# Kernel optimization log

Measured on AMD Instinct MI355X. Metric: run time of the kernel, lower is better.

The kernel has to match this reference:

```python
import jax, jax.numpy as jnp
import numpy as np
import math

N, E = 1000, 128000
IN_DIM, HID, OUT_DIM = 256, 512, 16
L, H = 6, 8
C = HID // H  # 64, TransformerConv out_channels per head
EDGE_DIM = 32
MAX_LEN = 1000


def _pe(max_len, d_model):
    pos = np.arange(max_len)[:, None].astype(np.float32)
    div = np.exp(np.arange(0, d_model, 2).astype(np.float32) * (-math.log(10000.0) / d_model))
    pe = np.zeros((max_len, d_model), dtype=np.float32)
    pe[:, 0::2] = np.sin(pos * div)
    pe[:, 1::2] = np.cos(pos * div)
    return jnp.asarray(pe)


def setup_inputs() -> dict:
    key = jax.random.key(0)
    ks = jax.random.split(key, 32)
    g = lambda k, shape, fan_in: jax.random.normal(k, shape, jnp.float32) / jnp.sqrt(jnp.float32(fan_in))
    inp = {
        "x": jax.random.normal(ks[0], (N, IN_DIM), jnp.float32),
        "edge_index": jax.random.randint(ks[1], (2, E), 0, N, jnp.int64 if jax.config.jax_enable_x64 else jnp.int32),
        "edge_attr": jax.random.uniform(ks[2], (E, 4), jnp.float32),
        "embed_w": g(ks[3], (IN_DIM, HID), IN_DIM),
        "embed_b": jnp.zeros((HID,), jnp.float32),
        "pe": _pe(MAX_LEN, HID),
        "ee_w1": g(ks[4], (4, 16), 4), "ee_b1": jnp.zeros((16,), jnp.float32),
        "ee_w2": g(ks[5], (16, EDGE_DIM), 16), "ee_b2": jnp.zeros((EDGE_DIM,), jnp.float32),
        "q_w": g(ks[6], (L, HID, HID), HID), "q_b": jnp.zeros((L, HID), jnp.float32),
        "k_w": g(ks[7], (L, HID, HID), HID), "k_b": jnp.zeros((L, HID), jnp.float32),
        "v_w": g(ks[8], (L, HID, HID), HID), "v_b": jnp.zeros((L, HID), jnp.float32),
        "e_w": g(ks[9], (L, EDGE_DIM, HID), EDGE_DIM),
        "skip_w": g(ks[10], (L, HID, HID), HID), "skip_b": jnp.zeros((L, HID), jnp.float32),
        "ln_g": jnp.ones((L, HID), jnp.float32), "ln_b": jnp.zeros((L, HID), jnp.float32),
        "dom_w": g(ks[11], (HID, 16), HID), "dom_b": jnp.zeros((16,), jnp.float32),
        "cls_w1": g(ks[12], (HID + 16, HID // 2), HID + 16), "cls_b1": jnp.zeros((HID // 2,), jnp.float32),
        "cls_w2": g(ks[13], (HID // 2, OUT_DIM), HID // 2), "cls_b2": jnp.zeros((OUT_DIM,), jnp.float32),
    }
    return inp


def _layer_norm(x, g, b, eps=1e-5):
    mu = jnp.mean(x, axis=-1, keepdims=True)
    var = jnp.var(x, axis=-1, keepdims=True)
    return (x - mu) * jax.lax.rsqrt(var + eps) * g + b


def _forward(x, edge_index, edge_attr, embed_w, embed_b, pe, ee_w1, ee_b1, ee_w2, ee_b2,
             q_w, q_b, k_w, k_b, v_w, v_b, e_w, skip_w, skip_b, ln_g, ln_b,
             dom_w, dom_b, cls_w1, cls_b1, cls_w2, cls_b2):
    n = x.shape[0]
    h = x @ embed_w + embed_b
    h = h + pe[:n]
    # edge encoder: 4 -> 16 -> 32
    ef = jax.nn.relu(edge_attr @ ee_w1 + ee_b1) @ ee_w2 + ee_b2  # [E, 32]
    src, tgt = edge_index[0], edge_index[1]
    scale = 1.0 / math.sqrt(C)
    for l in range(L):
        res = h
        q = (h @ q_w[l] + q_b[l]).reshape(n, H, C)
        k = (h @ k_w[l] + k_b[l]).reshape(n, H, C)
        v = (h @ v_w[l] + v_b[l]).reshape(n, H, C)
        e = (ef @ e_w[l]).reshape(-1, H, C)            # [E, H, C], lin_edge has no bias
        kj = k[src] + e                                 # gather + edge bias
        score = jnp.sum(q[tgt] * kj, axis=-1) * scale   # [E, H]
        # segment softmax over incoming edges of each target node
        m = jax.ops.segment_max(score, tgt, num_segments=n)     # [N, H]
        al = jnp.exp(score - m[tgt])
        den = jax.ops.segment_sum(al, tgt, num_segments=n)      # [N, H]
        al = al / den[tgt]
        msg = (v[src] + e) * al[:, :, None]             # [E, H, C]
        out = jax.ops.segment_sum(msg, tgt, num_segments=n).reshape(n, HID)
        out = out + h @ skip_w[l] + skip_b[l]           # root_weight skip
        h = _layer_norm(out + res, ln_g[l], ln_b[l])
    dom = h @ dom_w + dom_b                             # [N, 16]
    comb = jnp.concatenate([h, dom], axis=-1)
    hid = jax.nn.relu(comb @ cls_w1 + cls_b1)
    return hid @ cls_w2 + cls_b2


def reference(x, edge_index, edge_attr, embed_w, embed_b, pe, ee_w1, ee_b1, ee_w2, ee_b2,
              q_w, q_b, k_w, k_b, v_w, v_b, e_w, skip_w, skip_b, ln_g, ln_b,
              dom_w, dom_b, cls_w1, cls_b1, cls_w2, cls_b2):
    return _forward(x, edge_index, edge_attr, embed_w, embed_b, pe, ee_w1, ee_b1, ee_w2, ee_b2,
                    q_w, q_b, k_w, k_b, v_w, v_b, e_w, skip_w, skip_b, ln_g, ln_b,
                    dom_w, dom_b, cls_w1, cls_b1, cls_w2, cls_b2)
```

## Files before the change

### kernel.cpp

```cpp
#include <hip/hip_runtime.h>
#include <hip/hip_bf16.h>
#include <cstdint>
#include <cstddef>

#define NN 1000
#define EE 128000
#define LAYERS 6
#define SCALE 0.125f
#define MAXDEG 320

typedef __attribute__((ext_vector_type(4))) float f32x4;
typedef __attribute__((ext_vector_type(8))) short short8v;

static __device__ __forceinline__ unsigned short f2bf(float x){
    unsigned int u = __float_as_uint(x);
    unsigned int lsb = (u >> 16) & 1u;
    u += 0x7fffu + lsb;
    return (unsigned short)(u >> 16);
}
static __device__ __forceinline__ float bf2f(unsigned short u){
    return __uint_as_float(((unsigned int)u) << 16);
}

__global__ void zero_counts(int* cnt){
    cnt[threadIdx.x] = 0;
}

__global__ void hist_kernel(const int* __restrict__ tgt, int* cnt){
    int e = blockIdx.x*256 + threadIdx.x;
    if (e < EE) atomicAdd(&cnt[tgt[e]], 1);
}

__global__ void scan_kernel(const int* __restrict__ cnt, int* offs, int* cursor){
    __shared__ int s[1024];
    int tid = threadIdx.x;
    s[tid] = (tid < NN) ? cnt[tid] : 0;
    __syncthreads();
    for (int st = 1; st < 1024; st <<= 1){
        int v = (tid >= st) ? s[tid-st] : 0;
        __syncthreads();
        s[tid] += v;
        __syncthreads();
    }
    int excl = (tid == 0) ? 0 : s[tid-1];
    if (tid < NN){ offs[tid] = excl; cursor[tid] = excl; }
    if (tid == 0) offs[NN] = s[NN-1];
}

__global__ void scatter_kernel(const int* __restrict__ src, const int* __restrict__ tgt,
                               int* cursor, int* ssrc, int* epos){
    int e = blockIdx.x*256 + threadIdx.x;
    if (e < EE){
        int t = tgt[e];
        int pos = atomicAdd(&cursor[t], 1);
        ssrc[pos] = src[e];
        epos[e] = pos;
    }
}

__global__ __launch_bounds__(256) void edge_enc(
    const float* __restrict__ edge_attr,
    const float* __restrict__ w1, const float* __restrict__ b1,
    const float* __restrict__ w2, const float* __restrict__ b2,
    const int* __restrict__ epos,
    unsigned short* __restrict__ efs)
{
    __shared__ float w1s[64], b1s[16], w2s[512], b2s[32];
    int tid = threadIdx.x;
    if (tid < 64) w1s[tid] = w1[tid];
    if (tid < 16) b1s[tid] = b1[tid];
    if (tid < 32) b2s[tid] = b2[tid];
    w2s[tid] = w2[tid];
    w2s[tid+256] = w2[tid+256];
    __syncthreads();
    int e = blockIdx.x*256 + tid;
    if (e >= EE) return;
    float4 av = *(const float4*)(edge_attr + (size_t)e*4);
    float hd[16];
    #pragma unroll
    for (int i = 0; i < 16; i++){
        float v = av.x*w1s[i] + av.y*w1s[16+i] + av.z*w1s[32+i] + av.w*w1s[48+i] + b1s[i];
        hd[i] = fmaxf(v, 0.f);
    }
    unsigned short* op = efs + (size_t)epos[e]*32;
    #pragma unroll
    for (int k4 = 0; k4 < 8; k4++){
        ushort4 ub;
        float v0 = b2s[k4*4+0], v1 = b2s[k4*4+1], v2 = b2s[k4*4+2], v3 = b2s[k4*4+3];
        #pragma unroll
        for (int i = 0; i < 16; i++){
            float hv = hd[i];
            v0 += hv*w2s[i*32 + k4*4+0];
            v1 += hv*w2s[i*32 + k4*4+1];
            v2 += hv*w2s[i*32 + k4*4+2];
            v3 += hv*w2s[i*32 + k4*4+3];
        }
        ub.x = f2bf(v0); ub.y = f2bf(v1); ub.z = f2bf(v2); ub.w = f2bf(v3);
        *(ushort4*)(op + k4*4) = ub;
    }
}

__global__ __launch_bounds__(256) void convert_all(
    const float* __restrict__ Wq, const float* __restrict__ Wk,
    const float* __restrict__ Wv, const float* __restrict__ Ws,
    const float* __restrict__ embed_w, const float* __restrict__ x,
    unsigned short* __restrict__ Wt, unsigned short* __restrict__ ewt,
    unsigned short* __restrict__ xb)
{
    int bid = blockIdx.x;
    int tid = threadIdx.x;
    if (bid < 6144){
        int mm = bid >> 8;
        int tile = bid & 255;
        int tk = tile >> 4, tn = tile & 15;
        int l = mm >> 2, m = mm & 3;
        const float* W = ((m==0)?Wq:(m==1)?Wk:(m==2)?Wv:Ws) + (size_t)l*512*512;
        unsigned short* dst = Wt + (size_t)mm*512*512;
        __shared__ float ts[32][33];
        int r = tid >> 3, c0 = (tid & 7)*4;
        float4 v = *(const float4*)(W + (size_t)(tk*32 + r)*512 + tn*32 + c0);
        ts[r][c0+0] = v.x; ts[r][c0+1] = v.y; ts[r][c0+2] = v.z; ts[r][c0+3] = v.w;
        __syncthreads();
        ushort4 o;
        o.x = f2bf(ts[c0+0][r]); o.y = f2bf(ts[c0+1][r]);
        o.z = f2bf(ts[c0+2][r]); o.w = f2bf(ts[c0+3][r]);
        *(ushort4*)(dst + (size_t)(tn*32 + r)*512 + tk*32 + c0) = o;
    } else if (bid < 6144 + 128){
        int tile = bid - 6144;
        int tn = tile & 15, tk = tile >> 4;
        __shared__ float ts2[32][33];
        int r = tid >> 3, c0 = (tid & 7)*4;
        float4 v = *(const float4*)(embed_w + (size_t)(tk*32 + r)*512 + tn*32 + c0);
        ts2[r][c0+0] = v.x; ts2[r][c0+1] = v.y; ts2[r][c0+2] = v.z; ts2[r][c0+3] = v.w;
        __syncthreads();
        ushort4 o;
        o.x = f2bf(ts2[c0+0][r]); o.y = f2bf(ts2[c0+1][r]);
        o.z = f2bf(ts2[c0+2][r]); o.w = f2bf(ts2[c0+3][r]);
        *(ushort4*)(ewt + (size_t)(tn*32 + r)*256 + tk*32 + c0) = o;
    } else {
        int row = bid - 6144 - 128;
        xb[(size_t)row*256 + tid] = (row < NN) ? f2bf(x[(size_t)row*256 + tid]) : (unsigned short)0;
    }
}

__global__ __launch_bounds__(256) void gemm_embed_mfma(
    const unsigned short* __restrict__ xb,
    const unsigned short* __restrict__ ewt,
    const float* __restrict__ bias, const float* __restrict__ pe,
    float* __restrict__ C, unsigned short* __restrict__ hb)
{
    int bid = blockIdx.x;
    int mt = bid >> 2, nt = bid & 3;
    int row0 = mt*64, col0 = nt*128;

    __shared__ __align__(16) unsigned short As[64*40];
    __shared__ __align__(16) unsigned short Bs[128*40];

    int tid = threadIdx.x;
    int wid = tid >> 6, l = tid & 63;
    int wm = wid >> 1, wn = wid & 1;

    f32x4 acc[2][4] = {};
    int ar = tid >> 2, akq = tid & 3;
    for (int k0 = 0; k0 < 256; k0 += 32){
        *(uint4*)&As[ar*40 + akq*8]      = *(const uint4*)&xb[(size_t)(row0+ar)*256 + k0 + akq*8];
        *(uint4*)&Bs[ar*40 + akq*8]      = *(const uint4*)&ewt[(size_t)(col0+ar)*256 + k0 + akq*8];
        *(uint4*)&Bs[(ar+64)*40 + akq*8] = *(const uint4*)&ewt[(size_t)(col0+ar+64)*256 + k0 + akq*8];
        __syncthreads();
        short8v a0 = *(const short8v*)&As[(wm*32 + (l&15))*40 + (l>>4)*8];
        short8v a1 = *(const short8v*)&As[(wm*32 + 16 + (l&15))*40 + (l>>4)*8];
        #pragma unroll
        for (int nj = 0; nj < 4; nj++){
            short8v b = *(const short8v*)&Bs[(wn*64 + nj*16 + (l&15))*40 + (l>>4)*8];
            acc[0][nj] = __builtin_amdgcn_mfma_f32_16x16x32_bf16(a0, b, acc[0][nj], 0, 0, 0);
            acc[1][nj] = __builtin_amdgcn_mfma_f32_16x16x32_bf16(a1, b, acc[1][nj], 0, 0, 0);
        }
        __syncthreads();
    }
    int rbase = (l >> 4)*4, cl = l & 15;
    #pragma unroll
    for (int mi = 0; mi < 2; mi++)
        #pragma unroll
        for (int nj = 0; nj < 4; nj++)
            #pragma unroll
            for (int r = 0; r < 4; r++){
                int grow = row0 + wm*32 + mi*16 + rbase + r;
                int gcol = col0 + wn*64 + nj*16 + cl;
                if (grow < NN){
                    float v = acc[mi][nj][r] + bias[gcol] + pe[(size_t)grow*512 + gcol];
                    C[(size_t)grow*512 + gcol] = v;
                    hb[(size_t)grow*512 + gcol] = f2bf(v);
                }
            }
}

__global__ __launch_bounds__(256) void gemm_qkvs_mfma(
    const unsigned short* __restrict__ hb,
    const unsigned short* __restrict__ Wt,
    const float* __restrict__ qb, const float* __restrict__ kb,
    const float* __restrict__ vb, const float* __restrict__ sb,
    float* __restrict__ Q, unsigned short* __restrict__ K16,
    unsigned short* __restrict__ V16, float* __restrict__ S)
{
    int bid = blockIdx.x;
    int mat = bid >> 7;
    int rem = bid & 127;
    int mt = rem >> 3, nt = rem & 7;
    int row0 = mt*64, col0 = nt*64;
    const unsigned short* W = Wt + (size_t)mat*512*512;
    const float* bias = (mat==0)?qb:(mat==1)?kb:(mat==2)?vb:sb;

    __shared__ __align__(16) unsigned short As[64*72];
    __shared__ __align__(16) unsigned short Bs[64*72];

    int tid = threadIdx.x;
    int wid = tid >> 6, l = tid & 63;
    int wm = wid >> 1, wn = wid & 1;

    f32x4 acc[2][2] = {};
    int lr = tid >> 2;
    int lc = (tid & 3)*2;
    const unsigned short* ga = hb + (size_t)(row0+lr)*512 + lc*8;
    const unsigned short* gb = W  + (size_t)(col0+lr)*512 + lc*8;

    uint4 ra0 = *(const uint4*)(ga);
    uint4 ra1 = *(const uint4*)(ga + 8);
    uint4 rb0 = *(const uint4*)(gb);
    uint4 rb1 = *(const uint4*)(gb + 8);

    for (int k0 = 0; k0 < 512; k0 += 64){
        __syncthreads();
        *(uint4*)&As[lr*72 + lc*8]     = ra0;
        *(uint4*)&As[lr*72 + lc*8 + 8] = ra1;
        *(uint4*)&Bs[lr*72 + lc*8]     = rb0;
        *(uint4*)&Bs[lr*72 + lc*8 + 8] = rb1;
        __syncthreads();
        if (k0 + 64 < 512){
            ra0 = *(const uint4*)(ga + k0 + 64);
            ra1 = *(const uint4*)(ga + k0 + 72);
            rb0 = *(const uint4*)(gb + k0 + 64);
            rb1 = *(const uint4*)(gb + k0 + 72);
        }
        #pragma unroll
        for (int ks = 0; ks < 2; ks++){
            short8v a0 = *(const short8v*)&As[(wm*32 + (l&15))*72      + ks*32 + (l>>4)*8];
            short8v a1 = *(const short8v*)&As[(wm*32 + 16 + (l&15))*72 + ks*32 + (l>>4)*8];
            short8v b0 = *(const short8v*)&Bs[(wn*32 + (l&15))*72      + ks*32 + (l>>4)*8];
            short8v b1 = *(const short8v*)&Bs[(wn*32 + 16 + (l&15))*72 + ks*32 + (l>>4)*8];
            acc[0][0] = __builtin_amdgcn_mfma_f32_16x16x32_bf16(a0, b0, acc[0][0], 0, 0, 0);
            acc[0][1] = __builtin_amdgcn_mfma_f32_16x16x32_bf16(a0, b1, acc[0][1], 0, 0, 0);
            acc[1][0] = __builtin_amdgcn_mfma_f32_16x16x32_bf16(a1, b0, acc[1][0], 0, 0, 0);
            acc[1][1] = __builtin_amdgcn_mfma_f32_16x16x32_bf16(a1, b1, acc[1][1], 0, 0, 0);
        }
    }
    int rbase = (l >> 4)*4, cl = l & 15;
    #pragma unroll
    for (int mi = 0; mi < 2; mi++)
        #pragma unroll
        for (int nj = 0; nj < 2; nj++)
            #pragma unroll
            for (int r = 0; r < 4; r++){
                int grow = row0 + wm*32 + mi*16 + rbase + r;
                int gcol = col0 + wn*32 + nj*16 + cl;
                if (grow < NN){
                    float v = acc[mi][nj][r] + bias[gcol];
                    if (mat == 0)      Q[(size_t)grow*512 + gcol] = v;
                    else if (mat == 1) K16[(size_t)grow*512 + gcol] = f2bf(v);
                    else if (mat == 2) V16[(size_t)grow*512 + gcol] = f2bf(v);
                    else               S[(size_t)grow*512 + gcol] = v;
                }
            }
}

__global__ __launch_bounds__(256) void attn_h4(
    const float* __restrict__ Qm, const unsigned short* __restrict__ Km,
    const unsigned short* __restrict__ Vm,
    const unsigned short* __restrict__ efs, const float* __restrict__ e_w_l,
    const int* __restrict__ ssrc, const int* __restrict__ offs,
    float* __restrict__ x_pre)
{
    int tid = threadIdx.x;
    int b = blockIdx.x;
    int t = b >> 1;
    int hh0 = (b & 1)*4;

    __shared__ float q_s[4*68];
    __shared__ float qe_s[4*36];
    __shared__ float sc_s[MAXDEG*4];
    __shared__ int   src_s[MAXDEG];
    __shared__ float pv_s[4*256];
    __shared__ float pe_s[4*128];
    __shared__ float s_s[128];
    __shared__ float red[16], red2[16];
    __shared__ float m_s[4], d_s[4];

    q_s[(tid>>6)*68 + (tid&63)] = Qm[(size_t)t*512 + hh0*64 + tid];
    __syncthreads();
    if (tid < 128){
        int h = tid >> 5, d = tid & 31;
        const float* wrow = e_w_l + (size_t)d*512 + (hh0+h)*64;
        const float* qh = q_s + h*68;
        float a = 0.f;
        #pragma unroll
        for (int c = 0; c < 64; c++) a += qh[c]*wrow[c];
        qe_s[h*36 + d] = a;
    }
    int start = offs[t], deg = offs[t+1] - start;
    __syncthreads();

    int cw = tid >> 5, l = tid & 31;
    int h = l >> 3, sub = l & 7;
    const float4* qp4  = (const float4*)(q_s + h*68 + sub*8);
    float4 qa0 = qp4[0], qa1 = qp4[1];
    float4 qev = *(const float4*)(qe_s + h*36 + sub*4);
    float lmax = -1e30f;
    #pragma unroll 2
    for (int i = cw; i < deg; i += 8){
        int s = ssrc[start + i];
        if (l == 0) src_s[i] = s;
        short8v kv = *(const short8v*)(Km + (size_t)s*512 + (hh0 + h)*64 + sub*8);
        ushort4 ev = *(const ushort4*)(efs + (size_t)(start+i)*32 + sub*4);
        float p;
        p  = qa0.x*bf2f((unsigned short)kv[0]) + qa0.y*bf2f((unsigned short)kv[1])
           + qa0.z*bf2f((unsigned short)kv[2]) + qa0.w*bf2f((unsigned short)kv[3]);
        p += qa1.x*bf2f((unsigned short)kv[4]) + qa1.y*bf2f((unsigned short)kv[5])
           + qa1.z*bf2f((unsigned short)kv[6]) + qa1.w*bf2f((unsigned short)kv[7]);
        p += qev.x*bf2f(ev.x) + qev.y*bf2f(ev.y)
           + qev.z*bf2f(ev.z) + qev.w*bf2f(ev.w);
        p += __shfl_xor(p, 1);
        p += __shfl_xor(p, 2);
        p += __shfl_xor(p, 4);
        p *= SCALE;
        lmax = fmaxf(lmax, p);
        if (sub == 0) sc_s[i*4 + h] = p;
    }
    lmax = fmaxf(lmax, __shfl_xor(lmax, 32));
    {
        int wl = tid & 63;
        if (wl < 32 && (wl & 7) == 0) red[(tid>>6)*4 + (wl>>3)] = lmax;
    }
    __syncthreads();
    if (tid < 4){
        float m = fmaxf(fmaxf(red[tid], red[4+tid]), fmaxf(red[8+tid], red[12+tid]));
        m_s[tid] = m;
    }
    __syncthreads();

    {
        int he = tid & 3, ie = tid >> 2;
        float mh = m_s[he];
        float den = 0.f;
        for (int i = ie; i < deg; i += 64){
            float al = __expf(sc_s[i*4 + he] - mh);
            sc_s[i*4 + he] = al;
            den += al;
        }
        den += __shfl_xor(den, 4);
        den += __shfl_xor(den, 8);
        den += __shfl_xor(den, 16);
        den += __shfl_xor(den, 32);
        if ((tid & 63) < 4) red2[(tid>>6)*4 + (tid & 3)] = den;
    }
    __syncthreads();
    if (tid < 4) d_s[tid] = red2[tid] + red2[4+tid] + red2[8+tid] + red2[12+tid];
    __syncthreads();

    {
        int g = tid >> 6, c4 = tid & 63;
        int h2 = c4 >> 4;
        int dp = (c4 & 15)*2;
        float4 accV = make_float4(0.f,0.f,0.f,0.f);
        float2 accE = make_float2(0.f,0.f);
        #pragma unroll 4
        for (int i = g; i < deg; i += 4){
            int s = src_s[i];
            float al = sc_s[i*4 + h2];
            ushort4 v = *(const ushort4*)(Vm + (size_t)s*512 + hh0*64 + c4*4);
            unsigned int e2 = *(const unsigned int*)(efs + (size_t)(start+i)*32 + dp);
            accV.x += al*bf2f(v.x); accV.y += al*bf2f(v.y);
            accV.z += al*bf2f(v.z); accV.w += al*bf2f(v.w);
            accE.x += al*bf2f((unsigned short)(e2 & 0xffffu));
            accE.y += al*bf2f((unsigned short)(e2 >> 16));
        }
        *(float4*)&pv_s[g*256 + c4*4] = accV;
        *(float2*)&pe_s[g*128 + c4*2] = accE;
    }
    __syncthreads();
    if (tid < 128){
        int h3 = tid >> 5, d = tid & 31;
        int c4s = h3*16 + (d >> 1), comp = d & 1;
        float dv = d_s[h3];
        float invd = (dv > 0.f) ? 1.f/dv : 0.f;
        float ssum = pe_s[c4s*2+comp] + pe_s[128 + c4s*2+comp]
                   + pe_s[256 + c4s*2+comp] + pe_s[384 + c4s*2+comp];
        s_s[h3*32 + d] = ssum * invd;
    }
    __syncthreads();

    int c = tid;
    int hh = c >> 6;
    float dv = d_s[hh];
    float invd = (dv > 0.f) ? 1.f/dv : 0.f;
    float vtot = pv_s[c] + pv_s[256+c] + pv_s[512+c] + pv_s[768+c];
    float r = vtot * invd;
    float oe = 0.f;
    const float* sp = s_s + hh*32;
    #pragma unroll
    for (int d = 0; d < 32; d++) oe += sp[d]*e_w_l[(size_t)d*512 + hh0*64 + c];
    x_pre[(size_t)t*512 + hh0*64 + c] = r + oe;
}

__global__ __launch_bounds__(256) void ln_skip(
    const float* __restrict__ x_pre, const float* __restrict__ SKm,
    const float* __restrict__ hcur,
    const float* __restrict__ ln_g_l, const float* __restrict__ ln_b_l,
    float* __restrict__ hnext, unsigned short* __restrict__ hbn)
{
    int tid = threadIdx.x, t = blockIdx.x;
    __shared__ float red[4], red2[4];
    float x0 = x_pre[(size_t)t*512 + tid]       + SKm[(size_t)t*512 + tid]       + hcur[(size_t)t*512 + tid];
    float x1 = x_pre[(size_t)t*512 + 256 + tid] + SKm[(size_t)t*512 + 256 + tid] + hcur[(size_t)t*512 + 256 + tid];
    float sA = x0 + x1, sB = x0*x0 + x1*x1;
    #pragma unroll
    for (int m = 1; m <= 32; m <<= 1){
        sA += __shfl_xor(sA, m);
        sB += __shfl_xor(sB, m);
    }
    int wv = tid >> 6, ln = tid & 63;
    if (ln == 0){ red[wv] = sA; red2[wv] = sB; }
    __syncthreads();
    float tot  = red[0] + red[1] + red[2] + red[3];
    float tot2 = red2[0] + red2[1] + red2[2] + red2[3];
    float mu  = tot*(1.f/512.f);
    float var = tot2*(1.f/512.f) - mu*mu;
    float rstd = rsqrtf(var + 1e-5f);
    float y0 = (x0 - mu)*rstd*ln_g_l[tid]     + ln_b_l[tid];
    float y1 = (x1 - mu)*rstd*ln_g_l[256+tid] + ln_b_l[256+tid];
    hnext[(size_t)t*512 + tid]       = y0;
    hnext[(size_t)t*512 + 256 + tid] = y1;
    hbn[(size_t)t*512 + tid]       = f2bf(y0);
    hbn[(size_t)t*512 + 256 + tid] = f2bf(y1);
}

__global__ __launch_bounds__(256) void final_head(
    const float* __restrict__ hin,
    const float* __restrict__ dom_w, const float* __restrict__ dom_b,
    const float* __restrict__ w1, const float* __restrict__ b1,
    const float* __restrict__ w2, const float* __restrict__ b2,
    float* __restrict__ out)
{
    int tid = threadIdx.x, t = blockIdx.x;
    __shared__ float h_s[512];
    __shared__ float dom_s[16];
    __shared__ float hid_s[256];
    __shared__ float red[256];
    h_s[tid]     = hin[(size_t)t*512 + tid];
    h_s[tid+256] = hin[(size_t)t*512 + 256 + tid];
    __syncthreads();
    if (tid < 16){
        float a = dom_b[tid];
        for (int i = 0; i < 512; i++) a += h_s[i]*dom_w[i*16 + tid];
        dom_s[tid] = a;
    }
    __syncthreads();
    float acc = b1[tid];
    for (int i = 0; i < 512; i++) acc += h_s[i]*w1[(size_t)i*256 + tid];
    #pragma unroll
    for (int i = 0; i < 16; i++) acc += dom_s[i]*w1[(size_t)(512+i)*256 + tid];
    hid_s[tid] = fmaxf(acc, 0.f);
    __syncthreads();
    int o = tid & 15, g = tid >> 4;
    float p = 0.f;
    #pragma unroll
    for (int j = 0; j < 16; j++) p += hid_s[g*16 + j]*w2[(g*16 + j)*16 + o];
    red[tid] = p;
    __syncthreads();
    if (tid < 16){
        float s2 = b2[tid];
        for (int gg = 0; gg < 16; gg++) s2 += red[gg*16 + tid];
        out[(size_t)t*16 + tid] = s2;
    }
}

extern "C" void kernel_launch(void* const* d_in, const int* in_sizes, int n_in,
                              void* d_out, int out_size, void* d_ws, size_t ws_size,
                              hipStream_t stream)
{
    const float* x       = (const float*)d_in[0];
    const int*   eidx    = (const int*)  d_in[1];
    const float* eattr   = (const float*)d_in[2];
    const float* embed_w = (const float*)d_in[3];
    const float* embed_b = (const float*)d_in[4];
    const float* pe      = (const float*)d_in[5];
    const float* ee_w1   = (const float*)d_in[6];
    const float* ee_b1   = (const float*)d_in[7];
    const float* ee_w2   = (const float*)d_in[8];
    const float* ee_b2   = (const float*)d_in[9];
    const float* q_w     = (const float*)d_in[10];
    const float* q_b     = (const float*)d_in[11];
    const float* k_w     = (const float*)d_in[12];
    const float* k_b     = (const float*)d_in[13];
    const float* v_w     = (const float*)d_in[14];
    const float* v_b     = (const float*)d_in[15];
    const float* e_w     = (const float*)d_in[16];
    const float* skip_w  = (const float*)d_in[17];
    const float* skip_b  = (const float*)d_in[18];
    const float* ln_g    = (const float*)d_in[19];
    const float* ln_b    = (const float*)d_in[20];
    const float* dom_w   = (const float*)d_in[21];
    const float* dom_b   = (const float*)d_in[22];
    const float* cls_w1  = (const float*)d_in[23];
    const float* cls_b1  = (const float*)d_in[24];
    const float* cls_w2  = (const float*)d_in[25];
    const float* cls_b2  = (const float*)d_in[26];
    float* out = (float*)d_out;

    float* ws = (float*)d_ws;
    size_t o = 0;
    float* h0    = ws + o; o += (size_t)512*NN;
    float* h1    = ws + o; o += (size_t)512*NN;
    float* Qb    = ws + o; o += (size_t)512*NN;
    float* Sb    = ws + o; o += (size_t)512*NN;
    float* xpre  = ws + o; o += (size_t)512*NN;
    unsigned short* Kb16 = (unsigned short*)(ws + o); o += (size_t)1024*512/2;
    unsigned short* Vb16 = (unsigned short*)(ws + o); o += (size_t)1024*512/2;
    unsigned short* efs  = (unsigned short*)(ws + o); o += (size_t)EE*32/2;
    unsigned short* hb   = (unsigned short*)(ws + o); o += (size_t)1024*512/2;
    unsigned short* xb   = (unsigned short*)(ws + o); o += (size_t)1024*256/2;
    unsigned short* ewt  = (unsigned short*)(ws + o); o += (size_t)512*256/2;
    unsigned short* Wtb  = (unsigned short*)(ws + o); o += (size_t)24*512*512/2;
    int* cnt    = (int*)(ws + o); o += 1024;
    int* offs   = (int*)(ws + o); o += 1024;
    int* cursor = (int*)(ws + o); o += 1024;
    int* ssrc   = (int*)(ws + o); o += EE;
    int* epos   = (int*)(ws + o); o += EE;

    const int* srcp = eidx;
    const int* tgtp = eidx + EE;

    zero_counts<<<1, 1024, 0, stream>>>(cnt);
    hist_kernel<<<EE/256, 256, 0, stream>>>(tgtp, cnt);
    scan_kernel<<<1, 1024, 0, stream>>>(cnt, offs, cursor);
    scatter_kernel<<<EE/256, 256, 0, stream>>>(srcp, tgtp, cursor, ssrc, epos);
    edge_enc<<<EE/256, 256, 0, stream>>>(eattr, ee_w1, ee_b1, ee_w2, ee_b2, epos, efs);
    convert_all<<<6144 + 128 + 1024, 256, 0, stream>>>(q_w, k_w, v_w, skip_w, embed_w, x, Wtb, ewt, xb);
    gemm_embed_mfma<<<64, 256, 0, stream>>>(xb, ewt, embed_b, pe, h0, hb);

    float* hc = h0;
    float* hn = h1;
    for (int l = 0; l < LAYERS; l++){
        gemm_qkvs_mfma<<<512, 256, 0, stream>>>(
            hb, Wtb + (size_t)l*4*512*512,
            q_b + (size_t)l*512, k_b + (size_t)l*512,
            v_b + (size_t)l*512, skip_b + (size_t)l*512,
            Qb, Kb16, Vb16, Sb);
        attn_h4<<<2*NN, 256, 0, stream>>>(
            Qb, Kb16, Vb16, efs, e_w + (size_t)l*32*512,
            ssrc, offs, xpre);
        ln_skip<<<NN, 256, 0, stream>>>(
            xpre, Sb, hc,
            ln_g + (size_t)l*512, ln_b + (size_t)l*512,
            hn, hb);
        float* tmp = hc; hc = hn; hn = tmp;
    }
    final_head<<<NN, 256, 0, stream>>>(hc, dom_w, dom_b, cls_w1, cls_b1, cls_w2, cls_b2, out);
}
```

Before: 551.7 us.

## Compute attention scores with bf16 MFMA, one block per node over all heads

The attention kernel now handles all 8 heads of a target node in one block instead of splitting the heads over two blocks. Q·K scores are computed with 16x16x32 bf16 MFMA, using a block-diagonal B operand built from bf16 Q, and a second MFMA handles the edge-feature term. Softmax and the V and edge aggregation are reorganised to match. This halves the grid and is meant to replace scalar dot-product work with matrix instructions. The trade-offs are that Q is now rounded to bf16, most of each MFMA multiplies zeros, and there are fewer blocks for the GPU.

```diff
diff --git a/kernel.cpp b/kernel.cpp
--- a/kernel.cpp
+++ b/kernel.cpp
@@ -272,7 +272,7 @@
             }
 }
 
-__global__ __launch_bounds__(256) void attn_h4(
+__global__ __launch_bounds__(256) void attn_mfma(
     const float* __restrict__ Qm, const unsigned short* __restrict__ Km,
     const unsigned short* __restrict__ Vm,
     const unsigned short* __restrict__ efs, const float* __restrict__ e_w_l,
@@ -280,134 +280,158 @@
     float* __restrict__ x_pre)
 {
     int tid = threadIdx.x;
-    int b = blockIdx.x;
-    int t = b >> 1;
-    int hh0 = (b & 1)*4;
-
-    __shared__ float q_s[4*68];
-    __shared__ float qe_s[4*36];
-    __shared__ float sc_s[MAXDEG*4];
+    int t = blockIdx.x;
+
+    __shared__ float q_s[512];
+    __shared__ float qe_s[8*33];
+    __shared__ __align__(16) unsigned short qb_s[512];
+    __shared__ __align__(16) unsigned short qef_s[64*8];
+    __shared__ float sc_s[MAXDEG*8];
     __shared__ int   src_s[MAXDEG];
-    __shared__ float pv_s[4*256];
-    __shared__ float pe_s[4*128];
-    __shared__ float s_s[128];
-    __shared__ float red[16], red2[16];
-    __shared__ float m_s[4], d_s[4];
-
-    q_s[(tid>>6)*68 + (tid&63)] = Qm[(size_t)t*512 + hh0*64 + tid];
-    __syncthreads();
-    if (tid < 128){
-        int h = tid >> 5, d = tid & 31;
-        const float* wrow = e_w_l + (size_t)d*512 + (hh0+h)*64;
-        const float* qh = q_s + h*68;
+    __shared__ float pv_s[2][512];
+    __shared__ float pe_s[2][256];
+    __shared__ float s_s[256];
+    __shared__ float redm[32], redd[32];
+    __shared__ float m_s[8], d_s[8];
+
+    {
+        float v0 = Qm[(size_t)t*512 + tid];
+        float v1 = Qm[(size_t)t*512 + 256 + tid];
+        q_s[tid] = v0; q_s[256+tid] = v1;
+        qb_s[tid] = f2bf(v0); qb_s[256+tid] = f2bf(v1);
+    }
+    __syncthreads();
+    {
+        int hh = tid >> 5, dd = tid & 31;
+        const float* wrow = e_w_l + (size_t)dd*512 + hh*64;
+        const float* qh = q_s + hh*64;
         float a = 0.f;
         #pragma unroll
         for (int c = 0; c < 64; c++) a += qh[c]*wrow[c];
-        qe_s[h*36 + d] = a;
+        qe_s[hh*33 + dd] = a;
+    }
+    __syncthreads();
+    for (int idx = tid; idx < 512; idx += 256){
+        int l = idx >> 3, j = idx & 7;
+        int col = l & 15, d = (l >> 4)*8 + j;
+        float v = (col < 8) ? qe_s[col*33 + d] : 0.f;
+        qef_s[l*8 + j] = f2bf(v);
     }
     int start = offs[t], deg = offs[t+1] - start;
     __syncthreads();
 
-    int cw = tid >> 5, l = tid & 31;
-    int h = l >> 3, sub = l & 7;
-    const float4* qp4  = (const float4*)(q_s + h*68 + sub*8);
-    float4 qa0 = qp4[0], qa1 = qp4[1];
-    float4 qev = *(const float4*)(qe_s + h*36 + sub*4);
-    float lmax = -1e30f;
-    #pragma unroll 2
-    for (int i = cw; i < deg; i += 8){
-        int s = ssrc[start + i];
-        if (l == 0) src_s[i] = s;
-        short8v kv = *(const short8v*)(Km + (size_t)s*512 + (hh0 + h)*64 + sub*8);
-        ushort4 ev = *(const ushort4*)(efs + (size_t)(start+i)*32 + sub*4);
-        float p;
-        p  = qa0.x*bf2f((unsigned short)kv[0]) + qa0.y*bf2f((unsigned short)kv[1])
-           + qa0.z*bf2f((unsigned short)kv[2]) + qa0.w*bf2f((unsigned short)kv[3]);
-        p += qa1.x*bf2f((unsigned short)kv[4]) + qa1.y*bf2f((unsigned short)kv[5])
-           + qa1.z*bf2f((unsigned short)kv[6]) + qa1.w*bf2f((unsigned short)kv[7]);
-        p += qev.x*bf2f(ev.x) + qev.y*bf2f(ev.y)
-           + qev.z*bf2f(ev.z) + qev.w*bf2f(ev.w);
-        p += __shfl_xor(p, 1);
-        p += __shfl_xor(p, 2);
-        p += __shfl_xor(p, 4);
-        p *= SCALE;
-        lmax = fmaxf(lmax, p);
-        if (sub == 0) sc_s[i*4 + h] = p;
-    }
-    lmax = fmaxf(lmax, __shfl_xor(lmax, 32));
-    {
-        int wl = tid & 63;
-        if (wl < 32 && (wl & 7) == 0) red[(tid>>6)*4 + (wl>>3)] = lmax;
-    }
-    __syncthreads();
-    if (tid < 4){
-        float m = fmaxf(fmaxf(red[tid], red[4+tid]), fmaxf(red[8+tid], red[12+tid]));
-        m_s[tid] = m;
-    }
-    __syncthreads();
-
-    {
-        int he = tid & 3, ie = tid >> 2;
+    {
+        int wv = tid >> 6, l = tid & 63;
+        int arow = l & 15;
+        int achk = (l >> 4)*8;
+        const short8v bz = {0,0,0,0,0,0,0,0};
+        for (int eg = wv*16; eg < deg; eg += 64){
+            int e = eg + arow;
+            int ec = (e < deg) ? e : 0;
+            int s = ssrc[start + ec];
+            if (achk == 0 && e < deg) src_s[e] = s;
+            const unsigned short* kr = Km + (size_t)s*512 + achk;
+            f32x4 acc = {0.f, 0.f, 0.f, 0.f};
+            #pragma unroll
+            for (int ks = 0; ks < 16; ks++){
+                short8v a = *(const short8v*)(kr + ks*32);
+                short8v b = (arow == (ks >> 1)) ? *(const short8v*)(qb_s + ks*32 + achk) : bz;
+                acc = __builtin_amdgcn_mfma_f32_16x16x32_bf16(a, b, acc, 0, 0, 0);
+            }
+            {
+                short8v a = *(const short8v*)(efs + (size_t)(start+ec)*32 + achk);
+                short8v b = *(const short8v*)(qef_s + l*8);
+                acc = __builtin_amdgcn_mfma_f32_16x16x32_bf16(a, b, acc, 0, 0, 0);
+            }
+            #pragma unroll
+            for (int r = 0; r < 4; r++){
+                int er = eg + (l >> 4)*4 + r;
+                if (arow < 8 && er < deg) sc_s[er*8 + arow] = acc[r]*SCALE;
+            }
+        }
+    }
+    __syncthreads();
+
+    {
+        int he = tid & 7, ib = tid >> 3;
+        float lm = -1e30f;
+        for (int i = ib; i < deg; i += 32) lm = fmaxf(lm, sc_s[i*8 + he]);
+        lm = fmaxf(lm, __shfl_xor(lm, 8));
+        lm = fmaxf(lm, __shfl_xor(lm, 16));
+        lm = fmaxf(lm, __shfl_xor(lm, 32));
+        if ((tid & 63) < 8) redm[(tid>>6)*8 + (tid & 7)] = lm;
+    }
+    __syncthreads();
+    if (tid < 8) m_s[tid] = fmaxf(fmaxf(redm[tid], redm[8+tid]), fmaxf(redm[16+tid], redm[24+tid]));
+    __syncthreads();
+
+    {
+        int he = tid & 7, ib = tid >> 3;
         float mh = m_s[he];
         float den = 0.f;
-        for (int i = ie; i < deg; i += 64){
-            float al = __expf(sc_s[i*4 + he] - mh);
-            sc_s[i*4 + he] = al;
+        for (int i = ib; i < deg; i += 32){
+            float al = __expf(sc_s[i*8 + he] - mh);
+            sc_s[i*8 + he] = al;
             den += al;
         }
-        den += __shfl_xor(den, 4);
         den += __shfl_xor(den, 8);
         den += __shfl_xor(den, 16);
         den += __shfl_xor(den, 32);
-        if ((tid & 63) < 4) red2[(tid>>6)*4 + (tid & 3)] = den;
-    }
-    __syncthreads();
-    if (tid < 4) d_s[tid] = red2[tid] + red2[4+tid] + red2[8+tid] + red2[12+tid];
-    __syncthreads();
-
-    {
-        int g = tid >> 6, c4 = tid & 63;
-        int h2 = c4 >> 4;
-        int dp = (c4 & 15)*2;
-        float4 accV = make_float4(0.f,0.f,0.f,0.f);
-        float2 accE = make_float2(0.f,0.f);
-        #pragma unroll 4
-        for (int i = g; i < deg; i += 4){
+        if ((tid & 63) < 8) redd[(tid>>6)*8 + (tid & 7)] = den;
+    }
+    __syncthreads();
+    if (tid < 8) d_s[tid] = redd[tid] + redd[8+tid] + redd[16+tid] + redd[24+tid];
+    __syncthreads();
+
+    {
+        int g = tid >> 7, q7 = tid & 127;
+        int c4 = q7*4;
+        int h2 = c4 >> 6;
+        int hE = q7 >> 4, dE = (q7 & 15)*2;
+        float4 accV = make_float4(0.f, 0.f, 0.f, 0.f);
+        float2 accE = make_float2(0.f, 0.f);
+        #pragma unroll 2
+        for (int i = g; i < deg; i += 2){
             int s = src_s[i];
-            float al = sc_s[i*4 + h2];
-            ushort4 v = *(const ushort4*)(Vm + (size_t)s*512 + hh0*64 + c4*4);
-            unsigned int e2 = *(const unsigned int*)(efs + (size_t)(start+i)*32 + dp);
+            float al = sc_s[i*8 + h2];
+            float alE = sc_s[i*8 + hE];
+            ushort4 v = *(const ushort4*)(Vm + (size_t)s*512 + c4);
+            unsigned int e2 = *(const unsigned int*)(efs + (size_t)(start+i)*32 + dE);
             accV.x += al*bf2f(v.x); accV.y += al*bf2f(v.y);
             accV.z += al*bf2f(v.z); accV.w += al*bf2f(v.w);
-            accE.x += al*bf2f((unsigned short)(e2 & 0xffffu));
-            accE.y += al*bf2f((unsigned short)(e2 >> 16));
-        }
-        *(float4*)&pv_s[g*256 + c4*4] = accV;
-        *(float2*)&pe_s[g*128 + c4*2] = accE;
-    }
-    __syncthreads();
-    if (tid < 128){
-        int h3 = tid >> 5, d = tid & 31;
-        int c4s = h3*16 + (d >> 1), comp = d & 1;
-        float dv = d_s[h3];
+            accE.x += alE*bf2f((unsigned short)(e2 & 0xffffu));
+            accE.y += alE*bf2f((unsigned short)(e2 >> 16));
+        }
+        *(float4*)&pv_s[g][c4] = accV;
+        *(float2*)&pe_s[g][hE*32 + dE] = accE;
+    }
+    __syncthreads();
+    {
+        float dv = d_s[tid >> 5];
         float invd = (dv > 0.f) ? 1.f/dv : 0.f;
-        float ssum = pe_s[c4s*2+comp] + pe_s[128 + c4s*2+comp]
-                   + pe_s[256 + c4s*2+comp] + pe_s[384 + c4s*2+comp];
-        s_s[h3*32 + d] = ssum * invd;
-    }
-    __syncthreads();
-
-    int c = tid;
-    int hh = c >> 6;
-    float dv = d_s[hh];
-    float invd = (dv > 0.f) ? 1.f/dv : 0.f;
-    float vtot = pv_s[c] + pv_s[256+c] + pv_s[512+c] + pv_s[768+c];
-    float r = vtot * invd;
-    float oe = 0.f;
-    const float* sp = s_s + hh*32;
-    #pragma unroll
-    for (int d = 0; d < 32; d++) oe += sp[d]*e_w_l[(size_t)d*512 + hh0*64 + c];
-    x_pre[(size_t)t*512 + hh0*64 + c] = r + oe;
+        s_s[tid] = (pe_s[0][tid] + pe_s[1][tid]) * invd;
+    }
+    __syncthreads();
+
+    {
+        int c0 = tid, c1 = tid + 256;
+        int h0 = c0 >> 6, h1 = c1 >> 6;
+        float dv0 = d_s[h0], dv1 = d_s[h1];
+        float i0 = (dv0 > 0.f) ? 1.f/dv0 : 0.f;
+        float i1 = (dv1 > 0.f) ? 1.f/dv1 : 0.f;
+        float r0 = (pv_s[0][c0] + pv_s[1][c0]) * i0;
+        float r1 = (pv_s[0][c1] + pv_s[1][c1]) * i1;
+        float oe0 = 0.f, oe1 = 0.f;
+        const float* sp0 = s_s + h0*32;
+        const float* sp1 = s_s + h1*32;
+        #pragma unroll
+        for (int d = 0; d < 32; d++){
+            oe0 += sp0[d]*e_w_l[(size_t)d*512 + c0];
+            oe1 += sp1[d]*e_w_l[(size_t)d*512 + c1];
+        }
+        x_pre[(size_t)t*512 + c0] = r0 + oe0;
+        x_pre[(size_t)t*512 + c1] = r1 + oe1;
+    }
 }
 
 __global__ __launch_bounds__(256) void ln_skip(
@@ -554,7 +578,7 @@
             q_b + (size_t)l*512, k_b + (size_t)l*512,
             v_b + (size_t)l*512, skip_b + (size_t)l*512,
             Qb, Kb16, Vb16, Sb);
-        attn_h4<<<2*NN, 256, 0, stream>>>(
+        attn_mfma<<<NN, 256, 0, stream>>>(
             Qb, Kb16, Vb16, efs, e_w + (size_t)l*32*512,
             ssrc, offs, xpre);
         ln_skip<<<NN, 256, 0, stream>>>(
```

Result: slower. 581.8 us (+5.5%).
